# Kernel tuning notes

Measured on AMD Instinct MI355X. Metric: run time of the kernel, lower is better.

## Reference

```python
import jax, jax.numpy as jnp
import numpy as np

M0 = 0.5
M_MIN = 0.25
SCALE = 32.0
NUM_CLASSES = 100000
FEAT_DIM = 256
BATCH = 512


def setup_inputs() -> dict:
    key = jax.random.key(0)
    k1, k2, k3, k4 = jax.random.split(key, 4)
    features = jax.random.normal(k1, (BATCH, FEAT_DIM), dtype=jnp.float32)
    labels = jax.random.randint(k2, (BATCH,), 0, NUM_CLASSES, dtype=jnp.int64)
    weights = jax.random.uniform(k3, (BATCH,), dtype=jnp.float32)
    # xavier_uniform for (num_classes, feat_dim)
    limit = float(np.sqrt(6.0 / (NUM_CLASSES + FEAT_DIM)))
    weight = jax.random.uniform(k4, (NUM_CLASSES, FEAT_DIM), dtype=jnp.float32,
                                minval=-limit, maxval=limit)
    return {"features": features, "weight": weight, "weights": weights, "labels": labels}


def reference(features, weight, weights, labels):
    B = features.shape[0]
    norms = jnp.linalg.norm(features, axis=1)  # (B,)
    lo = jax.lax.stop_gradient(norms.min())
    hi = jax.lax.stop_gradient(norms.max())
    denom = jnp.maximum(hi - lo, 1e-8)
    margins = jnp.clip(M_MIN + (M0 - M_MIN) * (norms - lo) / denom, M_MIN, M0)  # (B,)

    feat_n = features / jnp.maximum(norms, 1e-12)[:, None]
    w_n = weight / jnp.maximum(jnp.linalg.norm(weight, axis=1), 1e-12)[:, None]
    cosine = jnp.clip(feat_n @ w_n.T, -1.0 + 1e-7, 1.0 - 1e-7)  # (B, C)

    rows = jnp.arange(B)
    cos_t = cosine[rows, labels]                      # target cosine (B,)
    theta_t = jnp.arccos(cos_t)
    cos_m_t = cos_t * jnp.cos(margins) - jnp.sin(theta_t) * jnp.sin(margins)

    logits = SCALE * cosine
    logits = logits.at[rows, labels].set(SCALE * cos_m_t)

    logp = jax.nn.log_softmax(logits, axis=1)
    per_sample = -logp[rows, labels]
    return (per_sample * weights).mean()
```

## Files before the change

### kernel.cpp

```cpp
#include <hip/hip_runtime.h>
#include <hip/hip_bf16.h>
#include <math.h>

#define BATCH 512
#define FEAT  256
#define NCLS  100000
#define SCALE_ 32.0f
#define M0_    0.5f
#define MMIN_  0.25f

#define BN 32
#define NT32 3125
#define NSLOTS 256
#define NPART 256
#define K4CHUNK 16
#define NK4 (NPART / K4CHUNK)

#define LOG2E_ 1.44269504088896f
#define K2C_   (SCALE_ * LOG2E_)

typedef unsigned short u16;
typedef short s16x8 __attribute__((ext_vector_type(8)));
typedef float f32x4 __attribute__((ext_vector_type(4)));

__device__ u16   g_fbf16[BATCH * FEAT];
__device__ float g_norms[BATCH];
__device__ float g_dot[BATCH];
__device__ float g_wn2[BATCH];
__device__ float g_psum[NPART * BATCH];
__device__ float g_qs[NK4 * BATCH];
__device__ int   g_lab32;

__device__ __forceinline__ u16 f2b(float x) {
  union { float f; unsigned u; } v; v.f = x;
  unsigned r = v.u + 0x7FFFu + ((v.u >> 16) & 1u);
  return (u16)(r >> 16);
}

__device__ __forceinline__ unsigned pkbf16(float a, float b) {
  unsigned r;
  asm("v_cvt_pk_bf16_f32 %0, %1, %2" : "=v"(r) : "v"(a), "v"(b));
  return r;
}

__device__ __forceinline__ float ex2(float x) {
  return __builtin_amdgcn_exp2f(x);
}

__global__ void k1a(const float* __restrict__ feat, const int* __restrict__ labw) {
  int wid = threadIdx.x >> 6, lane = threadIdx.x & 63;
  int row = blockIdx.x * 4 + wid;
  float4 f = ((const float4*)(feat + row * FEAT))[lane];
  float ss = f.x * f.x + f.y * f.y + f.z * f.z + f.w * f.w;
  #pragma unroll
  for (int d = 1; d < 64; d <<= 1) ss += __shfl_xor(ss, d, 64);
  float nrm = sqrtf(ss);
  float inv = 1.0f / fmaxf(nrm, 1e-12f);
  ushort4 h;
  h.x = f2b(f.x * inv); h.y = f2b(f.y * inv);
  h.z = f2b(f.z * inv); h.w = f2b(f.w * inv);
  ((ushort4*)(g_fbf16 + row * FEAT))[lane] = h;
  if (lane == 0) g_norms[row] = nrm;
  if (blockIdx.x == 0 && wid == 0) {
    int odd = 0;
    #pragma unroll
    for (int k = 0; k < 4; ++k) odd |= labw[2 * (k * 64 + lane) + 1];
    unsigned long long b = __ballot(odd != 0);
    if (lane == 0) g_lab32 = (b != 0ULL) ? 1 : 0;
  }
}

__global__ void k2c(const float* __restrict__ feat, const float* __restrict__ wmat,
                    const void* __restrict__ labels) {
  int wid = threadIdx.x >> 6, lane = threadIdx.x & 63;
  int i = blockIdx.x * 4 + wid;
  long long lab;
  if (g_lab32) lab = (long long)((const int*)labels)[i];
  else         lab = ((const long long*)labels)[i];
  float4 a = ((const float4*)(feat + i * FEAT))[lane];
  float4 b = ((const float4*)(wmat + (size_t)lab * FEAT))[lane];
  float d  = a.x * b.x + a.y * b.y + a.z * b.z + a.w * b.w;
  float bb = b.x * b.x + b.y * b.y + b.z * b.z + b.w * b.w;
  #pragma unroll
  for (int t = 1; t < 64; t <<= 1) {
    d  += __shfl_xor(d, t, 64);
    bb += __shfl_xor(bb, t, 64);
  }
  if (lane == 0) { g_dot[i] = d; g_wn2[i] = bb; }
}


#define LOADC(TILE) do {                                                    \
    rowL_ = tid >> 4;                                                       \
    int rg_ = (TILE) * BN + rowL_;                                          \
    const float4* src_ = (const float4*)(wmat + (size_t)rg_ * FEAT + (tid & 15) * 16); \
    v_[0] = src_[0]; v_[1] = src_[1]; v_[2] = src_[2]; v_[3] = src_[3];     \
  } while (0)

#define FINISHC(NB) do {                                                    \
    float ss_ = 0.0f;                                                       \
    _Pragma("unroll")                                                       \
    for (int k_ = 0; k_ < 4; ++k_)                                          \
      ss_ += v_[k_].x * v_[k_].x + v_[k_].y * v_[k_].y                      \
           + v_[k_].z * v_[k_].z + v_[k_].w * v_[k_].w;                     \
    ss_ += __shfl_xor(ss_, 1, 64);                                          \
    ss_ += __shfl_xor(ss_, 2, 64);                                          \
    ss_ += __shfl_xor(ss_, 4, 64);                                          \
    ss_ += __shfl_xor(ss_, 8, 64);                                          \
    float inv_ = 1.0f / fmaxf(sqrtf(ss_), 1e-12f);                          \
    u16* dst_ = &Ws[NB][0] + rowL_ * FEAT;                                  \
    _Pragma("unroll")                                                       \
    for (int k_ = 0; k_ < 2; ++k_) {                                        \
      int jj_ = (tid & 15) * 2 + k_;                                        \
      int4 w4_;                                                             \
      w4_.x = (int)pkbf16(v_[2*k_].x * inv_,   v_[2*k_].y * inv_);          \
      w4_.y = (int)pkbf16(v_[2*k_].z * inv_,   v_[2*k_].w * inv_);          \
      w4_.z = (int)pkbf16(v_[2*k_+1].x * inv_, v_[2*k_+1].y * inv_);        \
      w4_.w = (int)pkbf16(v_[2*k_+1].z * inv_, v_[2*k_+1].w * inv_);        \
      *(int4*)(dst_ + ((jj_ ^ (rowL_ & 7)) * 8)) = w4_;                     \
    }                                                                       \
  } while (0)

#define PHASE(p8) do {                                                      \
    f32x4 acc[2];                                                           \
    acc[0] = f32x4{0.0f, 0.0f, 0.0f, 0.0f};                                 \
    acc[1] = f32x4{0.0f, 0.0f, 0.0f, 0.0f};                                 \
    const u16* wb = &Ws[buf][0];                                            \
    const int row_ = (p8) * 16 + s;                                         \
    _Pragma("unroll")                                                       \
    for (int c = 0; c < 8; ++c) {                                           \
      int cc = c * 4 + q;                                                   \
      s16x8 wf = *(const s16x8*)(wb + row_ * FEAT + (cc ^ (row_ & 7)) * 8); \
      acc[0] = __builtin_amdgcn_mfma_f32_16x16x32_bf16(wf, fr[0][c], acc[0], 0, 0, 0); \
      acc[1] = __builtin_amdgcn_mfma_f32_16x16x32_bf16(wf, fr[1][c], acc[1], 0, 0, 0); \
    }                                                                       \
    _Pragma("unroll")                                                       \
    for (int m = 0; m < 2; ++m) {                                           \
      float sl = ex2(fmaf(acc[m][0], K2C_, -K2C_))                          \
               + ex2(fmaf(acc[m][1], K2C_, -K2C_))                          \
               + ex2(fmaf(acc[m][2], K2C_, -K2C_))                          \
               + ex2(fmaf(acc[m][3], K2C_, -K2C_));                         \
      S[m] += sl;                                                           \
    }                                                                       \
  } while (0)

__global__ __launch_bounds__(512, 2) void k3(const float* __restrict__ wmat) {
  __shared__ __align__(16) u16 Ws[2][BN * FEAT];

  const int tid  = threadIdx.x;
  const int lane = tid & 63, wid = tid >> 6;
  const int s = lane & 15, q = lane >> 4;
  const int bid = blockIdx.x;
  const int nslot = bid & 255;
  const int sh = bid >> 8;
  const int niter = ((NT32 - 1 - nslot) >> 8) + 1;

  int rowL_;
  float4 v_[4];

  LOADC(nslot); FINISHC(0);

  s16x8 fr[2][8];
  {
    const int srow = sh * 256 + wid * 32;
    #pragma unroll
    for (int m = 0; m < 2; ++m)
      #pragma unroll
      for (int c = 0; c < 8; ++c)
        fr[m][c] = *(const s16x8*)(g_fbf16 + (srow + m * 16 + s) * FEAT + c * 32 + q * 8);
  }

  float S[2] = {0.0f, 0.0f};

  __syncthreads();

  int buf = 0;
  for (int t = 0; t < niter; ++t) {
    const bool last = (t + 1 == niter);

    if (!last) LOADC(nslot + (t + 1) * NSLOTS);
    PHASE(0);
    if (!last) FINISHC(buf ^ 1);
    PHASE(1);
    __syncthreads();
    buf ^= 1;
  }

  #pragma unroll
  for (int m = 0; m < 2; ++m) {
    S[m] += __shfl_xor(S[m], 16, 64);
    S[m] += __shfl_xor(S[m], 32, 64);
  }

  if (lane < 16) {
    #pragma unroll
    for (int m = 0; m < 2; ++m) {
      int smp = sh * 256 + wid * 32 + m * 16 + lane;
      g_psum[nslot * BATCH + smp] = S[m];
    }
  }
}

__global__ __launch_bounds__(512) void k4a() {
  int i = threadIdx.x;
  int b = blockIdx.x;
  float S = 0.0f;
  #pragma unroll 4
  for (int p = b * K4CHUNK; p < b * K4CHUNK + K4CHUNK; ++p)
    S += g_psum[p * BATCH + i];
  g_qs[b * BATCH + i] = S;
}

__global__ void k4b(const float* __restrict__ wts, float* __restrict__ out) {
  int i = threadIdx.x;
  float S = 0.0f;
  #pragma unroll
  for (int t = 0; t < NK4; ++t) S += g_qs[t * BATCH + i];

  float n = g_norms[i];
  __shared__ float smin[512], smax[512];
  smin[i] = n; smax[i] = n;
  __syncthreads();
  for (int st = 256; st > 0; st >>= 1) {
    if (i < st) {
      smin[i] = fminf(smin[i], smin[i + st]);
      smax[i] = fmaxf(smax[i], smax[i + st]);
    }
    __syncthreads();
  }
  float lo = smin[0], hi = smax[0];
  float denom = fmaxf(hi - lo, 1e-8f);
  float mg = MMIN_ + (M0_ - MMIN_) * (n - lo) / denom;
  mg = fminf(fmaxf(mg, MMIN_), M0_);

  const float CLIP = 1.0f - 1e-7f;
  float wn = fmaxf(sqrtf(g_wn2[i]), 1e-12f);
  float ct = g_dot[i] / (fmaxf(n, 1e-12f) * wn);
  ct = fminf(fmaxf(ct, -CLIP), CLIP);

  float sint = sqrtf(fmaxf(0.0f, 1.0f - ct * ct));
  float cosm = ct * cosf(mg) - sint * sinf(mg);
  float b_old = K2C_ * ct;
  float b_new = K2C_ * cosm;
  float S2 = S - ex2(b_old - K2C_) + ex2(b_new - K2C_);
  float lse = 32.0f + logf(S2);
  float contrib = (lse - SCALE_ * cosm) * wts[i];
  __shared__ float sred[512];
  sred[i] = contrib;
  __syncthreads();
  for (int st = 256; st > 0; st >>= 1) {
    if (i < st) sred[i] += sred[i + st];
    __syncthreads();
  }
  if (i == 0) out[0] = sred[0] * (1.0f / (float)BATCH);
}

extern "C" void kernel_launch(void* const* d_in, const int* in_sizes, int n_in,
                              void* d_out, int out_size, void* d_ws, size_t ws_size,
                              hipStream_t stream) {
  const float* feat = (const float*)d_in[0];
  const float* wmat = (const float*)d_in[1];
  const float* wts  = (const float*)d_in[2];
  const void*  labs = d_in[3];
  float* out = (float*)d_out;

  hipLaunchKernelGGL(k1a, dim3(BATCH / 4), dim3(256), 0, stream, feat, (const int*)labs);
  hipLaunchKernelGGL(k2c, dim3(BATCH / 4), dim3(256), 0, stream, feat, wmat, labs);
  hipLaunchKernelGGL(k3,  dim3(512), dim3(512), 0, stream, wmat);
  hipLaunchKernelGGL(k4a, dim3(NK4), dim3(512), 0, stream);
  hipLaunchKernelGGL(k4b, dim3(1), dim3(512), 0, stream, wts, out);
}
```

Measured before the change: 60.11 us.

## Halve k3 block to 256 threads with 64 samples per wave

The main GEMM+softmax kernel now runs 4 waves per block instead of 8. Each wave holds 64 feature rows (4 MFMA accumulators) in registers rather than 32, and each thread loads and normalizes two weight rows per tile. The intent is more reuse of each LDS weight fragment per MFMA and less per-thread LDS traffic. In exchange, register pressure rises sharply (fr doubles to 64 VGPR-vectors) and launch bounds drop to one block of 256 threads, which may cut occupancy and latency hiding.

```diff
diff --git a/kernel.cpp b/kernel.cpp
--- a/kernel.cpp
+++ b/kernel.cpp
@@ -92,50 +92,59 @@
 
 #define LOADC(TILE) do {                                                    \
     rowL_ = tid >> 4;                                                       \
-    int rg_ = (TILE) * BN + rowL_;                                          \
-    const float4* src_ = (const float4*)(wmat + (size_t)rg_ * FEAT + (tid & 15) * 16); \
-    v_[0] = src_[0]; v_[1] = src_[1]; v_[2] = src_[2]; v_[3] = src_[3];     \
-  } while (0)
-
-#define FINISHC(NB) do {                                                    \
+    const float4* s0_ = (const float4*)(wmat + (size_t)((TILE) * BN + rowL_) * FEAT + (tid & 15) * 16);      \
+    const float4* s1_ = (const float4*)(wmat + (size_t)((TILE) * BN + 16 + rowL_) * FEAT + (tid & 15) * 16); \
+    v_[0] = s0_[0]; v_[1] = s0_[1]; v_[2] = s0_[2]; v_[3] = s0_[3];         \
+    v_[4] = s1_[0]; v_[5] = s1_[1]; v_[6] = s1_[2]; v_[7] = s1_[3];         \
+  } while (0)
+
+#define FINHALF(NB, G, ROW) do {                                            \
     float ss_ = 0.0f;                                                       \
     _Pragma("unroll")                                                       \
-    for (int k_ = 0; k_ < 4; ++k_)                                          \
-      ss_ += v_[k_].x * v_[k_].x + v_[k_].y * v_[k_].y                      \
-           + v_[k_].z * v_[k_].z + v_[k_].w * v_[k_].w;                     \
+    for (int k_ = 0; k_ < 4; ++k_) {                                        \
+      float4 vv_ = v_[(G) * 4 + k_];                                        \
+      ss_ += vv_.x * vv_.x + vv_.y * vv_.y + vv_.z * vv_.z + vv_.w * vv_.w; \
+    }                                                                       \
     ss_ += __shfl_xor(ss_, 1, 64);                                          \
     ss_ += __shfl_xor(ss_, 2, 64);                                          \
     ss_ += __shfl_xor(ss_, 4, 64);                                          \
     ss_ += __shfl_xor(ss_, 8, 64);                                          \
     float inv_ = 1.0f / fmaxf(sqrtf(ss_), 1e-12f);                          \
-    u16* dst_ = &Ws[NB][0] + rowL_ * FEAT;                                  \
+    u16* dst_ = &Ws[NB][0] + (ROW) * FEAT;                                  \
     _Pragma("unroll")                                                       \
     for (int k_ = 0; k_ < 2; ++k_) {                                        \
       int jj_ = (tid & 15) * 2 + k_;                                        \
+      float4 va_ = v_[(G) * 4 + 2 * k_], vb_ = v_[(G) * 4 + 2 * k_ + 1];    \
       int4 w4_;                                                             \
-      w4_.x = (int)pkbf16(v_[2*k_].x * inv_,   v_[2*k_].y * inv_);          \
-      w4_.y = (int)pkbf16(v_[2*k_].z * inv_,   v_[2*k_].w * inv_);          \
-      w4_.z = (int)pkbf16(v_[2*k_+1].x * inv_, v_[2*k_+1].y * inv_);        \
-      w4_.w = (int)pkbf16(v_[2*k_+1].z * inv_, v_[2*k_+1].w * inv_);        \
-      *(int4*)(dst_ + ((jj_ ^ (rowL_ & 7)) * 8)) = w4_;                     \
-    }                                                                       \
+      w4_.x = (int)pkbf16(va_.x * inv_, va_.y * inv_);                      \
+      w4_.y = (int)pkbf16(va_.z * inv_, va_.w * inv_);                      \
+      w4_.z = (int)pkbf16(vb_.x * inv_, vb_.y * inv_);                      \
+      w4_.w = (int)pkbf16(vb_.z * inv_, vb_.w * inv_);                      \
+      *(int4*)(dst_ + ((jj_ ^ ((ROW) & 7)) * 8)) = w4_;                     \
+    }                                                                       \
+  } while (0)
+
+#define FINISHC(NB) do {                                                    \
+    FINHALF(NB, 0, rowL_);                                                  \
+    FINHALF(NB, 1, 16 + rowL_);                                             \
   } while (0)
 
 #define PHASE(p8) do {                                                      \
-    f32x4 acc[2];                                                           \
-    acc[0] = f32x4{0.0f, 0.0f, 0.0f, 0.0f};                                 \
-    acc[1] = f32x4{0.0f, 0.0f, 0.0f, 0.0f};                                 \
+    f32x4 acc[4];                                                           \
+    _Pragma("unroll")                                                       \
+    for (int m = 0; m < 4; ++m) acc[m] = f32x4{0.0f, 0.0f, 0.0f, 0.0f};     \
     const u16* wb = &Ws[buf][0];                                            \
     const int row_ = (p8) * 16 + s;                                         \
     _Pragma("unroll")                                                       \
     for (int c = 0; c < 8; ++c) {                                           \
       int cc = c * 4 + q;                                                   \
       s16x8 wf = *(const s16x8*)(wb + row_ * FEAT + (cc ^ (row_ & 7)) * 8); \
-      acc[0] = __builtin_amdgcn_mfma_f32_16x16x32_bf16(wf, fr[0][c], acc[0], 0, 0, 0); \
-      acc[1] = __builtin_amdgcn_mfma_f32_16x16x32_bf16(wf, fr[1][c], acc[1], 0, 0, 0); \
-    }                                                                       \
-    _Pragma("unroll")                                                       \
-    for (int m = 0; m < 2; ++m) {                                           \
+      _Pragma("unroll")                                                     \
+      for (int m = 0; m < 4; ++m)                                           \
+        acc[m] = __builtin_amdgcn_mfma_f32_16x16x32_bf16(wf, fr[m][c], acc[m], 0, 0, 0); \
+    }                                                                       \
+    _Pragma("unroll")                                                       \
+    for (int m = 0; m < 4; ++m) {                                           \
       float sl = ex2(fmaf(acc[m][0], K2C_, -K2C_))                          \
                + ex2(fmaf(acc[m][1], K2C_, -K2C_))                          \
                + ex2(fmaf(acc[m][2], K2C_, -K2C_))                          \
@@ -144,7 +153,7 @@
     }                                                                       \
   } while (0)
 
-__global__ __launch_bounds__(512, 2) void k3(const float* __restrict__ wmat) {
+__global__ __launch_bounds__(256, 1) void k3(const float* __restrict__ wmat) {
   __shared__ __align__(16) u16 Ws[2][BN * FEAT];
 
   const int tid  = threadIdx.x;
@@ -156,21 +165,21 @@
   const int niter = ((NT32 - 1 - nslot) >> 8) + 1;
 
   int rowL_;
-  float4 v_[4];
+  float4 v_[8];
 
   LOADC(nslot); FINISHC(0);
 
-  s16x8 fr[2][8];
+  s16x8 fr[4][8];
   {
-    const int srow = sh * 256 + wid * 32;
+    const int srow = sh * 256 + wid * 64;
     #pragma unroll
-    for (int m = 0; m < 2; ++m)
+    for (int m = 0; m < 4; ++m)
       #pragma unroll
       for (int c = 0; c < 8; ++c)
         fr[m][c] = *(const s16x8*)(g_fbf16 + (srow + m * 16 + s) * FEAT + c * 32 + q * 8);
   }
 
-  float S[2] = {0.0f, 0.0f};
+  float S[4] = {0.0f, 0.0f, 0.0f, 0.0f};
 
   __syncthreads();
 
@@ -187,15 +196,15 @@
   }
 
   #pragma unroll
-  for (int m = 0; m < 2; ++m) {
+  for (int m = 0; m < 4; ++m) {
     S[m] += __shfl_xor(S[m], 16, 64);
     S[m] += __shfl_xor(S[m], 32, 64);
   }
 
   if (lane < 16) {
     #pragma unroll
-    for (int m = 0; m < 2; ++m) {
-      int smp = sh * 256 + wid * 32 + m * 16 + lane;
+    for (int m = 0; m < 4; ++m) {
+      int smp = sh * 256 + wid * 64 + m * 16 + lane;
       g_psum[nslot * BATCH + smp] = S[m];
     }
   }
@@ -266,7 +275,7 @@
 
   hipLaunchKernelGGL(k1a, dim3(BATCH / 4), dim3(256), 0, stream, feat, (const int*)labs);
   hipLaunchKernelGGL(k2c, dim3(BATCH / 4), dim3(256), 0, stream, feat, wmat, labs);
-  hipLaunchKernelGGL(k3,  dim3(512), dim3(512), 0, stream, wmat);
+  hipLaunchKernelGGL(k3,  dim3(512), dim3(256), 0, stream, wmat);
   hipLaunchKernelGGL(k4a, dim3(NK4), dim3(512), 0, stream);
   hipLaunchKernelGGL(k4b, dim3(1), dim3(512), 0, stream, wts, out);
 }
```

Result: no change. 59.42 us (-1.2%).
